# Kernel optimization log

Hardware: AMD Instinct MI355X
Metric: run time of the kernel (lower is better)

## Reference

```python
import jax, jax.numpy as jnp
from jax import lax
import numpy as np

C = 16          # channels
K = 3           # deformable kernel size
PAD = 1


def conv3(x, w, b):
    # 3x3 SAME conv, NCHW / OIHW
    y = lax.conv_general_dilated(x, w, (1, 1), 'SAME',
                                 dimension_numbers=('NCHW', 'OIHW', 'NCHW'))
    return y + b[None, :, None, None]


def deform_conv2d(x, offsets, mask, w, b):
    """torchvision-style modulated deformable conv, stride=1, pad=1, dil=1.
    x: [B,C,H,W]; offsets: [B,2*K*K,H,W] (per-tap y,x interleaved);
    mask: [B,K*K,H,W]; w: [Cout,C,K,K]; b: [Cout]."""
    B, Cin, H, W = x.shape
    ky, kx = jnp.meshgrid(jnp.arange(K), jnp.arange(K), indexing='ij')
    ky = ky.reshape(-1).astype(x.dtype)   # [9]
    kx = kx.reshape(-1).astype(x.dtype)
    off = offsets.reshape(B, K * K, 2, H, W)  # off[:,k,0]=dy, off[:,k,1]=dx
    hh = jnp.arange(H, dtype=x.dtype)
    ww = jnp.arange(W, dtype=x.dtype)
    py = hh[None, None, :, None] + (ky - PAD)[None, :, None, None] + off[:, :, 0]  # [B,9,H,W]
    px = ww[None, None, None, :] + (kx - PAD)[None, :, None, None] + off[:, :, 1]
    y0 = jnp.floor(py)
    x0 = jnp.floor(px)
    dy = py - y0
    dx = px - x0

    def sample_one(img, y0b, x0b, dyb, dxb):
        # img [C,H,W]; y0b/x0b/dyb/dxb [9,H,W]
        y0i = y0b.astype(jnp.int32)
        x0i = x0b.astype(jnp.int32)

        def gather(yi, xi):
            valid = ((yi >= 0) & (yi < H) & (xi >= 0) & (xi < W)).astype(img.dtype)
            yc = jnp.clip(yi, 0, H - 1)
            xc = jnp.clip(xi, 0, W - 1)
            return img[:, yc, xc] * valid[None]   # [C,9,H,W]

        v00 = gather(y0i,     x0i)
        v01 = gather(y0i,     x0i + 1)
        v10 = gather(y0i + 1, x0i)
        v11 = gather(y0i + 1, x0i + 1)
        return (v00 * (1 - dyb) * (1 - dxb) + v01 * (1 - dyb) * dxb
                + v10 * dyb * (1 - dxb) + v11 * dyb * dxb)   # [C,9,H,W]

    sampled = jax.vmap(sample_one)(x, y0, x0, dy, dx)          # [B,C,9,H,W]
    sampled = sampled * mask[:, None]                           # modulate
    out = jnp.einsum('bckhw,ock->bohw', sampled, w.reshape(w.shape[0], Cin, K * K))
    return out + b[None, :, None, None]


def setup_inputs() -> dict:
    key = jax.random.key(0)
    ks = iter(jax.random.split(key, 32))

    def w(shape, scale=0.1):
        return (jax.random.normal(next(ks), shape, dtype=jnp.float32) * scale)

    B, H, W = 4, 256, 256
    d = {
        'f_E': jax.random.normal(next(ks), (B, C, H, W), dtype=jnp.float32),
        'f_F': jax.random.normal(next(ks), (B, C, H, W), dtype=jnp.float32),
        # SpatialAttentionBlock
        'sab_att_w1': w((C, 2 * C, 3, 3)), 'sab_att_b1': w((C,)),
        'sab_att_w2': w((1, C, 3, 3)),      'sab_att_b2': w((1,)),
        'sab_ref_w':  w((C, 2 * C, 3, 3)),  'sab_ref_b':  w((C,)),
        # DeformableConvLayer offset/mask net (last layer small -> modest offsets)
        'om_w1': w((C, 2 * C, 3, 3)),       'om_b1': w((C,)),
        'om_w2': w((C, C, 3, 3)),           'om_b2': w((C,)),
        'om_w3': w((3 * K * K, C, 3, 3), 0.05), 'om_b3': w((3 * K * K,), 0.05),
        # deformable conv weight/bias
        'dcb_w': w((C, C, 3, 3)),           'dcb_b': w((C,)),
        # refinements
        'dcbref_w': w((C, 2 * C, 3, 3)),    'dcbref_b': w((C,)),
        'fin_w':    w((C, 2 * C, 3, 3)),    'fin_b':    w((C,)),
    }
    return d


def reference(f_E, f_F,
              sab_att_w1, sab_att_b1, sab_att_w2, sab_att_b2,
              sab_ref_w, sab_ref_b,
              om_w1, om_b1, om_w2, om_b2, om_w3, om_b3,
              dcb_w, dcb_b, dcbref_w, dcbref_b, fin_w, fin_b):
    relu = jax.nn.relu
    # --- SAB branch: sab(f_E, f_F) ---
    comb = jnp.concatenate([f_E, f_F], axis=1)
    M_E = jax.nn.sigmoid(conv3(relu(conv3(comb, sab_att_w1, sab_att_b1)),
                               sab_att_w2, sab_att_b2))          # [B,1,H,W]
    f_Esa = f_E * M_E
    f_EFsa = relu(conv3(jnp.concatenate([f_Esa, f_F], axis=1), sab_ref_w, sab_ref_b))
    # --- DCB branch: dcb_layer(f_F, f_E) -> deform on f_E, cat([f_E, f_F]) ---
    comb2 = jnp.concatenate([f_E, f_F], axis=1)
    om = conv3(relu(conv3(relu(conv3(comb2, om_w1, om_b1)), om_w2, om_b2)),
               om_w3, om_b3)                                      # [B,27,H,W]
    offsets = om[:, :2 * K * K]
    mask = jax.nn.sigmoid(om[:, 2 * K * K:])
    f_Edc = relu(deform_conv2d(f_E, offsets, mask, dcb_w, dcb_b))
    f_EFdc = relu(conv3(jnp.concatenate([f_Edc, f_F], axis=1), dcbref_w, dcbref_b))
    # --- final fusion ---
    f_EF = relu(conv3(jnp.concatenate([f_EFsa, f_EFdc], axis=1), fin_w, fin_b))
    return f_EF
```

## Files before the change

kernel.cpp:

```cpp
#include <hip/hip_runtime.h>
#include <cstdint>
#include <cstddef>

#define HH 256
#define WW 256
#define HWW (HH * WW)

typedef __attribute__((ext_vector_type(8))) short bf16x8;
typedef __attribute__((ext_vector_type(4))) float f32x4;

__device__ inline unsigned short f2bf(float f) {
  unsigned u = __float_as_uint(f);
  unsigned r = (u + 0x7fffu + ((u >> 16) & 1u)) >> 16;
  return (unsigned short)r;
}
__device__ inline float bf2f(unsigned short u) {
  return __uint_as_float((unsigned)u << 16);
}
__device__ inline float bf_lo(unsigned w) { return __uint_as_float(w << 16); }
__device__ inline float bf_hi(unsigned w) { return __uint_as_float(w & 0xffff0000u); }

struct RD { const float* src; void* dst; int cin, cout, mode; };
struct RA { RD d[9]; };

__global__ __launch_bounds__(256) void repack_k(RA a) {
  const RD t = a.d[blockIdx.x];
  if (t.mode == 2) {
    const int NST = (t.cin * 9 + 31) / 32;
    const int OT = (t.cout + 15) / 16;
    const int n = OT * NST * 512;
    unsigned short* dst = (unsigned short*)t.dst;
    for (int i = threadIdx.x; i < n; i += 256) {
      int j = i & 7;
      int l = (i >> 3) & 63;
      int rest = i >> 9;
      int s = rest % NST;
      int ot = rest / NST;
      int o = ot * 16 + (l & 15);
      int klin = s * 32 + ((l >> 4) << 3) + j;
      int tap = klin / t.cin;
      int c = klin % t.cin;
      float v = 0.f;
      if (tap < 9 && o < t.cout) v = t.src[(o * t.cin + c) * 9 + tap];
      dst[i] = f2bf(v);
    }
  } else {
    float* dst = (float*)t.dst;
    const int n = t.cin * t.cout * 9;
    for (int i = threadIdx.x; i < n; i += 256) {
      int k = i % 9;
      int rest = i / 9;
      int c = rest % t.cin;
      int o = rest / t.cin;
      if (t.mode == 0) dst[(c * 9 + k) * t.cout + o] = t.src[(o * t.cin + c) * 9 + k];
      else             dst[(k * t.cin + c) * t.cout + o] = t.src[(o * t.cin + c) * 9 + k];
    }
  }
}

__global__ __launch_bounds__(256) void nhwc2_k(
    const float* __restrict__ fe, const float* __restrict__ ff,
    unsigned short* __restrict__ xe, unsigned short* __restrict__ xf) {
  const int b = blockIdx.z;
  const int pixel = blockIdx.x * 256 + threadIdx.x;
#pragma unroll
  for (int t = 0; t < 2; ++t) {
    const float* src = t ? ff : fe;
    unsigned short* dst = t ? xf : xe;
    unsigned w[8];
#pragma unroll
    for (int j = 0; j < 8; ++j) {
      unsigned short lo = f2bf(src[((size_t)b * 16 + 2 * j) * HWW + pixel]);
      unsigned short hi = f2bf(src[((size_t)b * 16 + 2 * j + 1) * HWW + pixel]);
      w[j] = (unsigned)lo | ((unsigned)hi << 16);
    }
    uint4* d4 = (uint4*)(dst + ((size_t)b * HWW + pixel) * 16);
    d4[0] = make_uint4(w[0], w[1], w[2], w[3]);
    d4[1] = make_uint4(w[4], w[5], w[6], w[7]);
  }
}

template <int NSLOT, int OT, int OUT_MODE, int COUTR>
__global__ __launch_bounds__(256) void conv_nhwc(
    const unsigned short* __restrict__ inA, const unsigned short* __restrict__ inB,
    const unsigned short* __restrict__ wtm, const float* __restrict__ bias,
    void* __restrict__ outv) {
  constexpr int CIN = NSLOT * 8;
  constexpr int NST = (CIN * 9 + 31) / 32;
  constexpr int SHIFT = (NSLOT == 4) ? 1 : 2;
  constexpr int STRIDE = NSLOT * 16;
  constexpr int PX = 66, PY = 10;
  __shared__ __align__(16) char smem[PY * PX * STRIDE];

  const int b = blockIdx.z;
  const int tx0 = blockIdx.x * 64;
  const int ty0 = blockIdx.y * 8;
  const int tid = threadIdx.x;
  const int lane = tid & 63;
  const int wv = tid >> 6;

  bf16x8 afr[OT][NST];
#pragma unroll
  for (int ot = 0; ot < OT; ++ot)
#pragma unroll
    for (int s = 0; s < NST; ++s)
      afr[ot][s] = *(const bf16x8*)(wtm + (size_t)(((ot * NST + s) * 64 + lane) * 8));

  const int px_l = lane & 15;
  const int og = lane >> 4;

  f32x4 acc[8][OT];
#pragma unroll
  for (int ot = 0; ot < OT; ++ot) {
    f32x4 bv;
#pragma unroll
    for (int r = 0; r < 4; ++r) {
      int o = ot * 16 + og * 4 + r;
      bv[r] = bias[o < COUTR ? o : COUTR - 1];
    }
#pragma unroll
    for (int t = 0; t < 8; ++t) acc[t][ot] = bv;
  }

  for (int i = tid; i < PY * PX * NSLOT; i += 256) {
    int pp = i / NSLOT;
    int s = i - pp * NSLOT;
    int ly = pp / PX;
    int lx = pp - ly * PX;
    int gy = ty0 + ly - 1;
    int gx = tx0 + lx - 1;
    uint4 v = make_uint4(0, 0, 0, 0);
    if (gy >= 0 && gy < HH && gx >= 0 && gx < WW) {
      const unsigned short* src = (NSLOT == 2 || s < 2) ? inA : inB;
      int sl = (NSLOT == 4 && s >= 2) ? s - 2 : s;
      v = *(const uint4*)(src + ((size_t)b * HWW + (size_t)gy * WW + gx) * 16 + sl * 8);
    }
    int swz = (s ^ (pp >> SHIFT)) & (NSLOT - 1);
    *(uint4*)(smem + (size_t)pp * STRIDE + (swz << 4)) = v;
  }
  __syncthreads();

  int dpix[NST], dslot[NST];
#pragma unroll
  for (int s = 0; s < NST; ++s) {
    int klin = s * 32 + og * 8;
    int tap = klin / CIN;
    if (tap > 8) tap = 8;
    int coff = klin % CIN;
    dpix[s] = (tap / 3) * PX + (tap % 3);
    dslot[s] = coff >> 3;
  }

  const int oy_l = wv * 2;
#pragma unroll
  for (int t = 0; t < 8; ++t) {
    const int base_pix = (oy_l + (t >> 2)) * PX + (t & 3) * 16 + px_l;
#pragma unroll
    for (int s = 0; s < NST; ++s) {
      int pp = base_pix + dpix[s];
      int off = pp * STRIDE + (((dslot[s] ^ (pp >> SHIFT)) & (NSLOT - 1)) << 4);
      bf16x8 bvv = *(const bf16x8*)(smem + off);
#pragma unroll
      for (int ot = 0; ot < OT; ++ot)
        acc[t][ot] = __builtin_amdgcn_mfma_f32_16x16x32_bf16(afr[ot][s], bvv, acc[t][ot], 0, 0, 0);
    }
  }

#pragma unroll
  for (int t = 0; t < 8; ++t) {
    const int gy = ty0 + oy_l + (t >> 2);
    const int gx = tx0 + (t & 3) * 16 + px_l;
#pragma unroll
    for (int ot = 0; ot < OT; ++ot) {
      const int o0 = ot * 16 + og * 4;
      if (OUT_MODE == 2) {
        unsigned lo = (unsigned)f2bf(fmaxf(acc[t][ot][0], 0.f)) |
                      ((unsigned)f2bf(fmaxf(acc[t][ot][1], 0.f)) << 16);
        unsigned hi = (unsigned)f2bf(fmaxf(acc[t][ot][2], 0.f)) |
                      ((unsigned)f2bf(fmaxf(acc[t][ot][3], 0.f)) << 16);
        uint2* dst = (uint2*)((unsigned short*)outv +
                              ((size_t)b * HWW + (size_t)gy * WW + gx) * 16 + o0);
        *dst = make_uint2(lo, hi);
      } else if (OUT_MODE == 0) {
#pragma unroll
        for (int r = 0; r < 4; ++r) {
          int o = o0 + r;
          if (o < COUTR)
            ((float*)outv)[((size_t)b * COUTR + o) * HWW + (size_t)gy * WW + gx] =
                fmaxf(acc[t][ot][r], 0.f);
        }
      } else {
#pragma unroll
        for (int r = 0; r < 4; ++r) {
          int o = o0 + r;
          if (o < COUTR)
            ((unsigned short*)outv)[((size_t)b * COUTR + o) * HWW + (size_t)gy * WW + gx] =
                f2bf(acc[t][ot][r]);
        }
      }
    }
  }
}

__global__ __launch_bounds__(256) void conv_dual_k(
    const unsigned short* __restrict__ inA, const unsigned short* __restrict__ inB,
    const unsigned short* __restrict__ w1, const float* __restrict__ b1,
    const unsigned short* __restrict__ w2, const float* __restrict__ b2,
    unsigned short* __restrict__ out1, unsigned short* __restrict__ out2) {
  constexpr int NSLOT = 4, NST = 9, SHIFT = 1, STRIDE = 64, PX = 66, PY = 10;
  __shared__ __align__(16) char smem[PY * PX * STRIDE];

  const int b = blockIdx.z;
  const int tx0 = blockIdx.x * 64;
  const int ty0 = blockIdx.y * 8;
  const int tid = threadIdx.x;
  const int lane = tid & 63;
  const int wv = tid >> 6;

  bf16x8 afr1[NST], afr2[NST];
#pragma unroll
  for (int s = 0; s < NST; ++s) {
    afr1[s] = *(const bf16x8*)(w1 + (size_t)((s * 64 + lane) * 8));
    afr2[s] = *(const bf16x8*)(w2 + (size_t)((s * 64 + lane) * 8));
  }

  const int px_l = lane & 15;
  const int og = lane >> 4;

  f32x4 acc1[8], acc2[8];
  {
    f32x4 bv1, bv2;
#pragma unroll
    for (int r = 0; r < 4; ++r) {
      bv1[r] = b1[og * 4 + r];
      bv2[r] = b2[og * 4 + r];
    }
#pragma unroll
    for (int t = 0; t < 8; ++t) { acc1[t] = bv1; acc2[t] = bv2; }
  }

  for (int i = tid; i < PY * PX * NSLOT; i += 256) {
    int pp = i / NSLOT;
    int s = i - pp * NSLOT;
    int ly = pp / PX;
    int lx = pp - ly * PX;
    int gy = ty0 + ly - 1;
    int gx = tx0 + lx - 1;
    uint4 v = make_uint4(0, 0, 0, 0);
    if (gy >= 0 && gy < HH && gx >= 0 && gx < WW) {
      const unsigned short* src = (s < 2) ? inA : inB;
      int sl = (s >= 2) ? s - 2 : s;
      v = *(const uint4*)(src + ((size_t)b * HWW + (size_t)gy * WW + gx) * 16 + sl * 8);
    }
    int swz = (s ^ (pp >> SHIFT)) & 3;
    *(uint4*)(smem + (size_t)pp * STRIDE + (swz << 4)) = v;
  }
  __syncthreads();

  int dpix[NST], dslot[NST];
#pragma unroll
  for (int s = 0; s < NST; ++s) {
    int klin = s * 32 + og * 8;
    int tap = klin / 32;
    int coff = klin % 32;
    dpix[s] = (tap / 3) * PX + (tap % 3);
    dslot[s] = coff >> 3;
  }

  const int oy_l = wv * 2;
#pragma unroll
  for (int t = 0; t < 8; ++t) {
    const int base_pix = (oy_l + (t >> 2)) * PX + (t & 3) * 16 + px_l;
#pragma unroll
    for (int s = 0; s < NST; ++s) {
      int pp = base_pix + dpix[s];
      int off = pp * STRIDE + (((dslot[s] ^ (pp >> SHIFT)) & 3) << 4);
      bf16x8 bvv = *(const bf16x8*)(smem + off);
      acc1[t] = __builtin_amdgcn_mfma_f32_16x16x32_bf16(afr1[s], bvv, acc1[t], 0, 0, 0);
      acc2[t] = __builtin_amdgcn_mfma_f32_16x16x32_bf16(afr2[s], bvv, acc2[t], 0, 0, 0);
    }
  }

#pragma unroll
  for (int t = 0; t < 8; ++t) {
    const int gy = ty0 + oy_l + (t >> 2);
    const int gx = tx0 + (t & 3) * 16 + px_l;
    const int o0 = og * 4;
    size_t base = ((size_t)b * HWW + (size_t)gy * WW + gx) * 16 + o0;
    {
      unsigned lo = (unsigned)f2bf(fmaxf(acc1[t][0], 0.f)) |
                    ((unsigned)f2bf(fmaxf(acc1[t][1], 0.f)) << 16);
      unsigned hi = (unsigned)f2bf(fmaxf(acc1[t][2], 0.f)) |
                    ((unsigned)f2bf(fmaxf(acc1[t][3], 0.f)) << 16);
      *(uint2*)(out1 + base) = make_uint2(lo, hi);
    }
    {
      unsigned lo = (unsigned)f2bf(fmaxf(acc2[t][0], 0.f)) |
                    ((unsigned)f2bf(fmaxf(acc2[t][1], 0.f)) << 16);
      unsigned hi = (unsigned)f2bf(fmaxf(acc2[t][2], 0.f)) |
                    ((unsigned)f2bf(fmaxf(acc2[t][3], 0.f)) << 16);
      *(uint2*)(out2 + base) = make_uint2(lo, hi);
    }
  }
}

__global__ __launch_bounds__(256) void sagate_k(
    const unsigned short* __restrict__ xa, const unsigned short* __restrict__ xe,
    const unsigned short* __restrict__ xf,
    const float* __restrict__ gw, const float* __restrict__ gb,
    const unsigned short* __restrict__ wtm, const float* __restrict__ bias,
    unsigned short* __restrict__ out) {
  constexpr int NST = 9, SHIFT = 1, STRIDE = 64, PX = 66, PY = 10;
  __shared__ __align__(16) char smem[PY * PX * STRIDE];

  const int b = blockIdx.z;
  const int tx0 = blockIdx.x * 64;
  const int ty0 = blockIdx.y * 8;
  const int tid = threadIdx.x;
  const int lane = tid & 63;
  const int wv = tid >> 6;

  bf16x8 afr[NST];
#pragma unroll
  for (int s = 0; s < NST; ++s)
    afr[s] = *(const bf16x8*)(wtm + (size_t)((s * 64 + lane) * 8));

  const int px_l = lane & 15;
  const int og = lane >> 4;

  f32x4 acc[8];
  {
    f32x4 bv;
#pragma unroll
    for (int r = 0; r < 4; ++r) bv[r] = bias[og * 4 + r];
#pragma unroll
    for (int t = 0; t < 8; ++t) acc[t] = bv;
  }

  for (int i = tid; i < PY * PX * 2; i += 256) {
    int pp = i >> 1;
    int s = 2 + (i & 1);
    int ly = pp / PX;
    int lx = pp - ly * PX;
    int gy = ty0 + ly - 1;
    int gx = tx0 + lx - 1;
    uint4 v = make_uint4(0, 0, 0, 0);
    if (gy >= 0 && gy < HH && gx >= 0 && gx < WW)
      v = *(const uint4*)(xf + ((size_t)b * HWW + (size_t)gy * WW + gx) * 16 + (s - 2) * 8);
    int swz = (s ^ (pp >> SHIFT)) & 3;
    *(uint4*)(smem + (size_t)pp * STRIDE + (swz << 4)) = v;
  }

  const float gbias = gb[0];
  for (int i = tid; i < PY * PX; i += 256) {
    int ly = i / PX;
    int lx = i - ly * PX;
    int gy = ty0 + ly - 1;
    int gx = tx0 + lx - 1;
    uint4 v0 = make_uint4(0, 0, 0, 0), v1 = make_uint4(0, 0, 0, 0);
    if (gy >= 0 && gy < HH && gx >= 0 && gx < WW) {
      float a = gbias;
#pragma unroll
      for (int ky = 0; ky < 3; ++ky) {
        int ay = gy + ky - 1;
        if (ay < 0 || ay >= HH) continue;
#pragma unroll
        for (int kx = 0; kx < 3; ++kx) {
          int ax = gx + kx - 1;
          if (ax < 0 || ax >= WW) continue;
          const int k = ky * 3 + kx;
          const uint4* p = (const uint4*)(xa + ((size_t)b * HWW + (size_t)ay * WW + ax) * 16);
          uint4 t0 = p[0], t1 = p[1];
          unsigned wv8[8] = {t0.x, t0.y, t0.z, t0.w, t1.x, t1.y, t1.z, t1.w};
#pragma unroll
          for (int j = 0; j < 8; ++j) {
            a = fmaf(bf_lo(wv8[j]), gw[(2 * j) * 9 + k], a);
            a = fmaf(bf_hi(wv8[j]), gw[(2 * j + 1) * 9 + k], a);
          }
        }
      }
      float m = 1.0f / (1.0f + expf(-a));
      const uint4* pe = (const uint4*)(xe + ((size_t)b * HWW + (size_t)gy * WW + gx) * 16);
      uint4 e0 = pe[0], e1 = pe[1];
      unsigned ev[8] = {e0.x, e0.y, e0.z, e0.w, e1.x, e1.y, e1.z, e1.w};
      unsigned r[8];
#pragma unroll
      for (int j = 0; j < 8; ++j) {
        unsigned short lo = f2bf(bf_lo(ev[j]) * m);
        unsigned short hi = f2bf(bf_hi(ev[j]) * m);
        r[j] = (unsigned)lo | ((unsigned)hi << 16);
      }
      v0 = make_uint4(r[0], r[1], r[2], r[3]);
      v1 = make_uint4(r[4], r[5], r[6], r[7]);
    }
    int swz0 = (0 ^ (i >> SHIFT)) & 3;
    int swz1 = (1 ^ (i >> SHIFT)) & 3;
    *(uint4*)(smem + (size_t)i * STRIDE + (swz0 << 4)) = v0;
    *(uint4*)(smem + (size_t)i * STRIDE + (swz1 << 4)) = v1;
  }
  __syncthreads();

  int dpix[NST], dslot[NST];
#pragma unroll
  for (int s = 0; s < NST; ++s) {
    int klin = s * 32 + og * 8;
    int tap = klin / 32;
    int coff = klin % 32;
    dpix[s] = (tap / 3) * PX + (tap % 3);
    dslot[s] = coff >> 3;
  }

  const int oy_l = wv * 2;
#pragma unroll
  for (int t = 0; t < 8; ++t) {
    const int base_pix = (oy_l + (t >> 2)) * PX + (t & 3) * 16 + px_l;
#pragma unroll
    for (int s = 0; s < NST; ++s) {
      int pp = base_pix + dpix[s];
      int off = pp * STRIDE + (((dslot[s] ^ (pp >> SHIFT)) & 3) << 4);
      bf16x8 bvv = *(const bf16x8*)(smem + off);
      acc[t] = __builtin_amdgcn_mfma_f32_16x16x32_bf16(afr[s], bvv, acc[t], 0, 0, 0);
    }
  }

#pragma unroll
  for (int t = 0; t < 8; ++t) {
    const int gy = ty0 + oy_l + (t >> 2);
    const int gx = tx0 + (t & 3) * 16 + px_l;
    const int o0 = og * 4;
    unsigned lo = (unsigned)f2bf(fmaxf(acc[t][0], 0.f)) |
                  ((unsigned)f2bf(fmaxf(acc[t][1], 0.f)) << 16);
    unsigned hi = (unsigned)f2bf(fmaxf(acc[t][2], 0.f)) |
                  ((unsigned)f2bf(fmaxf(acc[t][3], 0.f)) << 16);
    *(uint2*)(out + ((size_t)b * HWW + (size_t)gy * WW + gx) * 16 + o0) = make_uint2(lo, hi);
  }
}

__global__ __launch_bounds__(256) void deform_v4(
    const unsigned short* __restrict__ xn, const unsigned short* __restrict__ om,
    const float* __restrict__ wt, const float* __restrict__ bias,
    unsigned short* __restrict__ out) {
  const int bid = blockIdx.x;
  const int xcd = bid & 7;
  const int b = xcd >> 1;
  const int pb = ((bid >> 3) << 1) | (xcd & 1);
  const int pixel = pb * 256 + (int)threadIdx.x;
  const int y = pixel >> 8;
  const int xq = pixel & 255;
  const unsigned short* xb = xn + (size_t)b * HWW * 16;
  const unsigned short* omb = om + (size_t)b * 27 * HWW;

  float acc[16];
#pragma unroll
  for (int o = 0; o < 16; ++o) acc[o] = bias[o];

#pragma unroll
  for (int k = 0; k < 9; ++k) {
    float offy = bf2f(omb[(size_t)(2 * k) * HWW + pixel]);
    float offx = bf2f(omb[(size_t)(2 * k + 1) * HWW + pixel]);
    float m = 1.0f / (1.0f + expf(-bf2f(omb[(size_t)(18 + k) * HWW + pixel])));
    float py = (float)y + (float)(k / 3 - 1) + offy;
    float px = (float)xq + (float)(k % 3 - 1) + offx;
    float y0f = floorf(py);
    float x0f = floorf(px);
    float dy = py - y0f;
    float dx = px - x0f;
    int y0 = (int)y0f, x0 = (int)x0f;
    int y1 = y0 + 1, x1 = x0 + 1;
    bool vy0 = (y0 >= 0) && (y0 < HH);
    bool vy1 = (y1 >= 0) && (y1 < HH);
    bool vx0 = (x0 >= 0) && (x0 < WW);
    bool vx1 = (x1 >= 0) && (x1 < WW);
    int yc0 = min(max(y0, 0), HH - 1);
    int yc1 = min(max(y1, 0), HH - 1);
    int xc0 = min(max(x0, 0), WW - 1);
    int xc1 = min(max(x1, 0), WW - 1);
    float w00 = (1.f - dy) * (1.f - dx) * m;
    float w01 = (1.f - dy) * dx * m;
    float w10 = dy * (1.f - dx) * m;
    float w11 = dy * dx * m;
    if (!(vy0 && vx0)) w00 = 0.f;
    if (!(vy0 && vx1)) w01 = 0.f;
    if (!(vy1 && vx0)) w10 = 0.f;
    if (!(vy1 && vx1)) w11 = 0.f;

    const uint4* p00 = (const uint4*)(xb + (size_t)(yc0 * WW + xc0) * 16);
    const uint4* p01 = (const uint4*)(xb + (size_t)(yc0 * WW + xc1) * 16);
    const uint4* p10 = (const uint4*)(xb + (size_t)(yc1 * WW + xc0) * 16);
    const uint4* p11 = (const uint4*)(xb + (size_t)(yc1 * WW + xc1) * 16);
    uint4 a0 = p00[0], a1 = p00[1];
    uint4 b0 = p01[0], b1 = p01[1];
    uint4 c0 = p10[0], c1 = p10[1];
    uint4 d0 = p11[0], d1 = p11[1];
    unsigned wA[8] = {a0.x, a0.y, a0.z, a0.w, a1.x, a1.y, a1.z, a1.w};
    unsigned wB[8] = {b0.x, b0.y, b0.z, b0.w, b1.x, b1.y, b1.z, b1.w};
    unsigned wC[8] = {c0.x, c0.y, c0.z, c0.w, c1.x, c1.y, c1.z, c1.w};
    unsigned wD[8] = {d0.x, d0.y, d0.z, d0.w, d1.x, d1.y, d1.z, d1.w};

    float s[16];
#pragma unroll
    for (int j = 0; j < 8; ++j) {
      s[2 * j]     = bf_lo(wA[j]) * w00 + bf_lo(wB[j]) * w01 + bf_lo(wC[j]) * w10 + bf_lo(wD[j]) * w11;
      s[2 * j + 1] = bf_hi(wA[j]) * w00 + bf_hi(wB[j]) * w01 + bf_hi(wC[j]) * w10 + bf_hi(wD[j]) * w11;
    }
    const float* wk = wt + (size_t)k * 256;
#pragma unroll
    for (int c = 0; c < 16; ++c)
#pragma unroll
      for (int o = 0; o < 16; ++o)
        acc[o] = fmaf(s[c], wk[c * 16 + o], acc[o]);
  }
  unsigned r[8];
#pragma unroll
  for (int j = 0; j < 8; ++j) {
    unsigned short lo = f2bf(fmaxf(acc[2 * j], 0.f));
    unsigned short hi = f2bf(fmaxf(acc[2 * j + 1], 0.f));
    r[j] = (unsigned)lo | ((unsigned)hi << 16);
  }
  uint4* d4 = (uint4*)(out + ((size_t)b * HWW + pixel) * 16);
  d4[0] = make_uint4(r[0], r[1], r[2], r[3]);
  d4[1] = make_uint4(r[4], r[5], r[6], r[7]);
}

extern "C" void kernel_launch(void* const* d_in, const int* in_sizes, int n_in,
                              void* d_out, int out_size, void* d_ws, size_t ws_size,
                              hipStream_t stream) {
  (void)in_sizes; (void)n_in; (void)out_size; (void)ws_size;
  const float* f_E = (const float*)d_in[0];
  const float* f_F = (const float*)d_in[1];
  const float* att_w1 = (const float*)d_in[2];
  const float* att_b1 = (const float*)d_in[3];
  const float* att_w2 = (const float*)d_in[4];
  const float* att_b2 = (const float*)d_in[5];
  const float* ref_w = (const float*)d_in[6];
  const float* ref_b = (const float*)d_in[7];
  const float* om_w1 = (const float*)d_in[8];
  const float* om_b1 = (const float*)d_in[9];
  const float* om_w2 = (const float*)d_in[10];
  const float* om_b2 = (const float*)d_in[11];
  const float* om_w3 = (const float*)d_in[12];
  const float* om_b3 = (const float*)d_in[13];
  const float* dcb_w = (const float*)d_in[14];
  const float* dcb_b = (const float*)d_in[15];
  const float* dcbref_w = (const float*)d_in[16];
  const float* dcbref_b = (const float*)d_in[17];
  const float* fin_w = (const float*)d_in[18];
  const float* fin_b = (const float*)d_in[19];
  float* outp = (float*)d_out;

  const size_t TN = (size_t)4 * HWW * 16;
  unsigned short* XE  = (unsigned short*)d_ws;
  unsigned short* XF  = XE + TN;
  unsigned short* XA  = XF + TN;
  unsigned short* XT  = XA + TN;
  unsigned short* X2  = XT + TN;
  unsigned short* XSA = X2 + TN;
  unsigned short* OMB = XSA + TN;
  unsigned short* WM  = OMB + (size_t)4 * 27 * HWW;

  unsigned short* WM_att1 = WM;
  unsigned short* WM_ref  = WM_att1 + 4608;
  unsigned short* WM_om1  = WM_ref + 4608;
  unsigned short* WM_om2  = WM_om1 + 4608;
  unsigned short* WM_om3  = WM_om2 + 2560;
  unsigned short* WM_dref = WM_om3 + 5120;
  unsigned short* WM_fin  = WM_dref + 4608;
  float* WF_att2 = (float*)(WM_fin + 4608);
  float* WF_dcb  = WF_att2 + 144;

  RA ra;
  ra.d[0] = {att_w1, WM_att1, 32, 16, 2};
  ra.d[1] = {ref_w, WM_ref, 32, 16, 2};
  ra.d[2] = {om_w1, WM_om1, 32, 16, 2};
  ra.d[3] = {om_w2, WM_om2, 16, 16, 2};
  ra.d[4] = {om_w3, WM_om3, 16, 27, 2};
  ra.d[5] = {dcbref_w, WM_dref, 32, 16, 2};
  ra.d[6] = {fin_w, WM_fin, 32, 16, 2};
  ra.d[7] = {att_w2, WF_att2, 16, 1, 0};
  ra.d[8] = {dcb_w, WF_dcb, 16, 16, 1};
  repack_k<<<dim3(9), dim3(256), 0, stream>>>(ra);
  nhwc2_k<<<dim3(HWW / 256, 1, 4), dim3(256), 0, stream>>>(f_E, f_F, XE, XF);

  dim3 blk(256);
  dim3 gm(WW / 64, HH / 8, 4);

  conv_dual_k<<<gm, blk, 0, stream>>>(XE, XF, WM_att1, att_b1, WM_om1, om_b1, XA, XT);
  sagate_k<<<gm, blk, 0, stream>>>(XA, XE, XF, WF_att2, att_b2, WM_ref, ref_b, X2);
  conv_nhwc<2, 1, 2, 16><<<gm, blk, 0, stream>>>(XT, nullptr, WM_om2, om_b2, XA);
  conv_nhwc<2, 2, 1, 27><<<gm, blk, 0, stream>>>(XA, nullptr, WM_om3, om_b3, OMB);
  deform_v4<<<dim3(1024), blk, 0, stream>>>(XE, OMB, WF_dcb, dcb_b, XSA);
  conv_nhwc<4, 1, 2, 16><<<gm, blk, 0, stream>>>(XSA, XF, WM_dref, dcbref_b, XT);
  conv_nhwc<4, 1, 0, 16><<<gm, blk, 0, stream>>>(X2, XT, WM_fin, fin_b, outp);
}
```

Measured before the change: 121.8 us.

## Use zero-padded NHWC buffers and direct global loads in convs

Switches all intermediate NHWC bf16 tensors to a zero-bordered 258x258 layout, with a small kernel that clears the borders. The conv kernels can then read halo pixels straight from global memory with no bounds checks, dropping the LDS staging and barrier. Block indices are remapped so adjacent blocks are spread across batch and tiles, which is meant to improve cache locality. The cost is that the nine overlapping tap reads now depend on L1/L2 reuse instead of shared memory, so global load traffic goes up.

```diff
diff --git a/kernel.cpp b/kernel.cpp
--- a/kernel.cpp
+++ b/kernel.cpp
@@ -5,6 +5,7 @@
 #define HH 256
 #define WW 256
 #define HWW (HH * WW)
+#define PS 258
 
 typedef __attribute__((ext_vector_type(8))) short bf16x8;
 typedef __attribute__((ext_vector_type(4))) float f32x4;
@@ -58,11 +59,30 @@
   }
 }
 
+struct BorderP { unsigned short* p[6]; };
+
+__global__ __launch_bounds__(256) void border_k(BorderP bp) {
+  unsigned short* t = bp.p[blockIdx.x];
+  const int b = blockIdx.y;
+  for (int i = threadIdx.x; i < 1028; i += 256) {
+    int row, col;
+    if (i < 258) { row = 0; col = i; }
+    else if (i < 516) { row = 257; col = i - 258; }
+    else if (i < 772) { row = i - 516 + 1; col = 0; }
+    else { row = i - 772 + 1; col = 257; }
+    uint4* d = (uint4*)(t + ((size_t)(b * PS + row) * PS + col) * 16);
+    d[0] = make_uint4(0, 0, 0, 0);
+    d[1] = make_uint4(0, 0, 0, 0);
+  }
+}
+
 __global__ __launch_bounds__(256) void nhwc2_k(
     const float* __restrict__ fe, const float* __restrict__ ff,
     unsigned short* __restrict__ xe, unsigned short* __restrict__ xf) {
   const int b = blockIdx.z;
   const int pixel = blockIdx.x * 256 + threadIdx.x;
+  const int y = pixel >> 8;
+  const int x = pixel & 255;
 #pragma unroll
   for (int t = 0; t < 2; ++t) {
     const float* src = t ? ff : fe;
@@ -74,27 +94,26 @@
       unsigned short hi = f2bf(src[((size_t)b * 16 + 2 * j + 1) * HWW + pixel]);
       w[j] = (unsigned)lo | ((unsigned)hi << 16);
     }
-    uint4* d4 = (uint4*)(dst + ((size_t)b * HWW + pixel) * 16);
+    uint4* d4 = (uint4*)(dst + ((size_t)(b * PS + y + 1) * PS + x + 1) * 16);
     d4[0] = make_uint4(w[0], w[1], w[2], w[3]);
     d4[1] = make_uint4(w[4], w[5], w[6], w[7]);
   }
 }
 
 template <int NSLOT, int OT, int OUT_MODE, int COUTR>
-__global__ __launch_bounds__(256) void conv_nhwc(
+__global__ __launch_bounds__(256) void conv_direct(
     const unsigned short* __restrict__ inA, const unsigned short* __restrict__ inB,
     const unsigned short* __restrict__ wtm, const float* __restrict__ bias,
     void* __restrict__ outv) {
   constexpr int CIN = NSLOT * 8;
   constexpr int NST = (CIN * 9 + 31) / 32;
-  constexpr int SHIFT = (NSLOT == 4) ? 1 : 2;
-  constexpr int STRIDE = NSLOT * 16;
-  constexpr int PX = 66, PY = 10;
-  __shared__ __align__(16) char smem[PY * PX * STRIDE];
-
-  const int b = blockIdx.z;
-  const int tx0 = blockIdx.x * 64;
-  const int ty0 = blockIdx.y * 8;
+
+  const int bid = blockIdx.x;
+  const int wg = (bid & 7) * 64 + (bid >> 3);
+  const int b = wg >> 7;
+  const int rem = wg & 127;
+  const int ty0 = (rem >> 2) * 8;
+  const int tx0 = (rem & 3) * 64;
   const int tid = threadIdx.x;
   const int lane = tid & 63;
   const int wv = tid >> 6;
@@ -122,48 +141,38 @@
     for (int t = 0; t < 8; ++t) acc[t][ot] = bv;
   }
 
-  for (int i = tid; i < PY * PX * NSLOT; i += 256) {
-    int pp = i / NSLOT;
-    int s = i - pp * NSLOT;
-    int ly = pp / PX;
-    int lx = pp - ly * PX;
-    int gy = ty0 + ly - 1;
-    int gx = tx0 + lx - 1;
-    uint4 v = make_uint4(0, 0, 0, 0);
-    if (gy >= 0 && gy < HH && gx >= 0 && gx < WW) {
-      const unsigned short* src = (NSLOT == 2 || s < 2) ? inA : inB;
-      int sl = (NSLOT == 4 && s >= 2) ? s - 2 : s;
-      v = *(const uint4*)(src + ((size_t)b * HWW + (size_t)gy * WW + gx) * 16 + sl * 8);
-    }
-    int swz = (s ^ (pp >> SHIFT)) & (NSLOT - 1);
-    *(uint4*)(smem + (size_t)pp * STRIDE + (swz << 4)) = v;
-  }
-  __syncthreads();
-
-  int dpix[NST], dslot[NST];
+  int offE[NST];
+  bool useB[NST];
 #pragma unroll
   for (int s = 0; s < NST; ++s) {
     int klin = s * 32 + og * 8;
     int tap = klin / CIN;
     if (tap > 8) tap = 8;
     int coff = klin % CIN;
-    dpix[s] = (tap / 3) * PX + (tap % 3);
-    dslot[s] = coff >> 3;
+    int slot = (NSLOT == 4) ? (coff >> 3) & 1 : (coff >> 3);
+    useB[s] = (NSLOT == 4) && (coff >= 16);
+    offE[s] = ((tap / 3) * PS + (tap % 3)) * 16 + slot * 8;
   }
 
   const int oy_l = wv * 2;
 #pragma unroll
   for (int t = 0; t < 8; ++t) {
-    const int base_pix = (oy_l + (t >> 2)) * PX + (t & 3) * 16 + px_l;
+    const int gy = ty0 + oy_l + (t >> 2);
+    const int gx = tx0 + (t & 3) * 16 + px_l;
+    const size_t base = ((size_t)(b * PS + gy) * PS + gx) * 16;
+    const unsigned short* baseA = inA + base;
+    const unsigned short* baseB = inB + base;
+    bf16x8 bv[NST];
 #pragma unroll
     for (int s = 0; s < NST; ++s) {
-      int pp = base_pix + dpix[s];
-      int off = pp * STRIDE + (((dslot[s] ^ (pp >> SHIFT)) & (NSLOT - 1)) << 4);
-      bf16x8 bvv = *(const bf16x8*)(smem + off);
+      const unsigned short* p = useB[s] ? baseB : baseA;
+      bv[s] = *(const bf16x8*)(p + offE[s]);
+    }
+#pragma unroll
+    for (int s = 0; s < NST; ++s)
 #pragma unroll
       for (int ot = 0; ot < OT; ++ot)
-        acc[t][ot] = __builtin_amdgcn_mfma_f32_16x16x32_bf16(afr[ot][s], bvv, acc[t][ot], 0, 0, 0);
-    }
+        acc[t][ot] = __builtin_amdgcn_mfma_f32_16x16x32_bf16(afr[ot][s], bv[s], acc[t][ot], 0, 0, 0);
   }
 
 #pragma unroll
@@ -179,7 +188,7 @@
         unsigned hi = (unsigned)f2bf(fmaxf(acc[t][ot][2], 0.f)) |
                       ((unsigned)f2bf(fmaxf(acc[t][ot][3], 0.f)) << 16);
         uint2* dst = (uint2*)((unsigned short*)outv +
-                              ((size_t)b * HWW + (size_t)gy * WW + gx) * 16 + o0);
+                              ((size_t)(b * PS + gy + 1) * PS + gx + 1) * 16 + o0);
         *dst = make_uint2(lo, hi);
       } else if (OUT_MODE == 0) {
 #pragma unroll
@@ -202,17 +211,18 @@
   }
 }
 
-__global__ __launch_bounds__(256) void conv_dual_k(
+__global__ __launch_bounds__(256) void conv_dual_direct(
     const unsigned short* __restrict__ inA, const unsigned short* __restrict__ inB,
     const unsigned short* __restrict__ w1, const float* __restrict__ b1,
     const unsigned short* __restrict__ w2, const float* __restrict__ b2,
     unsigned short* __restrict__ out1, unsigned short* __restrict__ out2) {
-  constexpr int NSLOT = 4, NST = 9, SHIFT = 1, STRIDE = 64, PX = 66, PY = 10;
-  __shared__ __align__(16) char smem[PY * PX * STRIDE];
-
-  const int b = blockIdx.z;
-  const int tx0 = blockIdx.x * 64;
-  const int ty0 = blockIdx.y * 8;
+  constexpr int NST = 9;
+  const int bid = blockIdx.x;
+  const int wg = (bid & 7) * 64 + (bid >> 3);
+  const int b = wg >> 7;
+  const int rem = wg & 127;
+  const int ty0 = (rem >> 2) * 8;
+  const int tx0 = (rem & 3) * 64;
   const int tid = threadIdx.x;
   const int lane = tid & 63;
   const int wv = tid >> 6;
@@ -239,54 +249,44 @@
     for (int t = 0; t < 8; ++t) { acc1[t] = bv1; acc2[t] = bv2; }
   }
 
-  for (int i = tid; i < PY * PX * NSLOT; i += 256) {
-    int pp = i / NSLOT;
-    int s = i - pp * NSLOT;
-    int ly = pp / PX;
-    int lx = pp - ly * PX;
-    int gy = ty0 + ly - 1;
-    int gx = tx0 + lx - 1;
-    uint4 v = make_uint4(0, 0, 0, 0);
-    if (gy >= 0 && gy < HH && gx >= 0 && gx < WW) {
-      const unsigned short* src = (s < 2) ? inA : inB;
-      int sl = (s >= 2) ? s - 2 : s;
-      v = *(const uint4*)(src + ((size_t)b * HWW + (size_t)gy * WW + gx) * 16 + sl * 8);
-    }
-    int swz = (s ^ (pp >> SHIFT)) & 3;
-    *(uint4*)(smem + (size_t)pp * STRIDE + (swz << 4)) = v;
-  }
-  __syncthreads();
-
-  int dpix[NST], dslot[NST];
+  int offE[NST];
+  bool useB[NST];
 #pragma unroll
   for (int s = 0; s < NST; ++s) {
     int klin = s * 32 + og * 8;
     int tap = klin / 32;
     int coff = klin % 32;
-    dpix[s] = (tap / 3) * PX + (tap % 3);
-    dslot[s] = coff >> 3;
+    int slot = (coff >> 3) & 1;
+    useB[s] = (coff >= 16);
+    offE[s] = ((tap / 3) * PS + (tap % 3)) * 16 + slot * 8;
   }
 
   const int oy_l = wv * 2;
-#pragma unroll
-  for (int t = 0; t < 8; ++t) {
-    const int base_pix = (oy_l + (t >> 2)) * PX + (t & 3) * 16 + px_l;
-#pragma unroll
-    for (int s = 0; s < NST; ++s) {
-      int pp = base_pix + dpix[s];
-      int off = pp * STRIDE + (((dslot[s] ^ (pp >> SHIFT)) & 3) << 4);
-      bf16x8 bvv = *(const bf16x8*)(smem + off);
-      acc1[t] = __builtin_amdgcn_mfma_f32_16x16x32_bf16(afr1[s], bvv, acc1[t], 0, 0, 0);
-      acc2[t] = __builtin_amdgcn_mfma_f32_16x16x32_bf16(afr2[s], bvv, acc2[t], 0, 0, 0);
-    }
-  }
-
 #pragma unroll
   for (int t = 0; t < 8; ++t) {
     const int gy = ty0 + oy_l + (t >> 2);
     const int gx = tx0 + (t & 3) * 16 + px_l;
-    const int o0 = og * 4;
-    size_t base = ((size_t)b * HWW + (size_t)gy * WW + gx) * 16 + o0;
+    const size_t base = ((size_t)(b * PS + gy) * PS + gx) * 16;
+    const unsigned short* baseA = inA + base;
+    const unsigned short* baseB = inB + base;
+    bf16x8 bv[NST];
+#pragma unroll
+    for (int s = 0; s < NST; ++s) {
+      const unsigned short* p = useB[s] ? baseB : baseA;
+      bv[s] = *(const bf16x8*)(p + offE[s]);
+    }
+#pragma unroll
+    for (int s = 0; s < NST; ++s) {
+      acc1[t] = __builtin_amdgcn_mfma_f32_16x16x32_bf16(afr1[s], bv[s], acc1[t], 0, 0, 0);
+      acc2[t] = __builtin_amdgcn_mfma_f32_16x16x32_bf16(afr2[s], bv[s], acc2[t], 0, 0, 0);
+    }
+  }
+
+#pragma unroll
+  for (int t = 0; t < 8; ++t) {
+    const int gy = ty0 + oy_l + (t >> 2);
+    const int gx = tx0 + (t & 3) * 16 + px_l;
+    const size_t base = ((size_t)(b * PS + gy + 1) * PS + gx + 1) * 16 + og * 4;
     {
       unsigned lo = (unsigned)f2bf(fmaxf(acc1[t][0], 0.f)) |
                     ((unsigned)f2bf(fmaxf(acc1[t][1], 0.f)) << 16);
@@ -342,11 +342,7 @@
     int s = 2 + (i & 1);
     int ly = pp / PX;
     int lx = pp - ly * PX;
-    int gy = ty0 + ly - 1;
-    int gx = tx0 + lx - 1;
-    uint4 v = make_uint4(0, 0, 0, 0);
-    if (gy >= 0 && gy < HH && gx >= 0 && gx < WW)
-      v = *(const uint4*)(xf + ((size_t)b * HWW + (size_t)gy * WW + gx) * 16 + (s - 2) * 8);
+    uint4 v = *(const uint4*)(xf + ((size_t)(b * PS + ty0 + ly) * PS + tx0 + lx) * 16 + (s - 2) * 8);
     int swz = (s ^ (pp >> SHIFT)) & 3;
     *(uint4*)(smem + (size_t)pp * STRIDE + (swz << 4)) = v;
   }
@@ -355,48 +351,41 @@
   for (int i = tid; i < PY * PX; i += 256) {
     int ly = i / PX;
     int lx = i - ly * PX;
-    int gy = ty0 + ly - 1;
-    int gx = tx0 + lx - 1;
-    uint4 v0 = make_uint4(0, 0, 0, 0), v1 = make_uint4(0, 0, 0, 0);
-    if (gy >= 0 && gy < HH && gx >= 0 && gx < WW) {
-      float a = gbias;
-#pragma unroll
-      for (int ky = 0; ky < 3; ++ky) {
-        int ay = gy + ky - 1;
-        if (ay < 0 || ay >= HH) continue;
-#pragma unroll
-        for (int kx = 0; kx < 3; ++kx) {
-          int ax = gx + kx - 1;
-          if (ax < 0 || ax >= WW) continue;
-          const int k = ky * 3 + kx;
-          const uint4* p = (const uint4*)(xa + ((size_t)b * HWW + (size_t)ay * WW + ax) * 16);
-          uint4 t0 = p[0], t1 = p[1];
-          unsigned wv8[8] = {t0.x, t0.y, t0.z, t0.w, t1.x, t1.y, t1.z, t1.w};
-#pragma unroll
-          for (int j = 0; j < 8; ++j) {
-            a = fmaf(bf_lo(wv8[j]), gw[(2 * j) * 9 + k], a);
-            a = fmaf(bf_hi(wv8[j]), gw[(2 * j + 1) * 9 + k], a);
-          }
+    const int pcy = ty0 + ly;
+    const int pcx = tx0 + lx;
+    float a = gbias;
+#pragma unroll
+    for (int ky = 0; ky < 3; ++ky) {
+      int ty = min(max(pcy + ky - 1, 0), PS - 1);
+#pragma unroll
+      for (int kx = 0; kx < 3; ++kx) {
+        int tx = min(max(pcx + kx - 1, 0), PS - 1);
+        const int k = ky * 3 + kx;
+        const uint4* p = (const uint4*)(xa + ((size_t)(b * PS + ty) * PS + tx) * 16);
+        uint4 t0 = p[0], t1 = p[1];
+        unsigned wv8[8] = {t0.x, t0.y, t0.z, t0.w, t1.x, t1.y, t1.z, t1.w};
+#pragma unroll
+        for (int j = 0; j < 8; ++j) {
+          a = fmaf(bf_lo(wv8[j]), gw[(2 * j) * 9 + k], a);
+          a = fmaf(bf_hi(wv8[j]), gw[(2 * j + 1) * 9 + k], a);
         }
       }
-      float m = 1.0f / (1.0f + expf(-a));
-      const uint4* pe = (const uint4*)(xe + ((size_t)b * HWW + (size_t)gy * WW + gx) * 16);
-      uint4 e0 = pe[0], e1 = pe[1];
-      unsigned ev[8] = {e0.x, e0.y, e0.z, e0.w, e1.x, e1.y, e1.z, e1.w};
-      unsigned r[8];
-#pragma unroll
-      for (int j = 0; j < 8; ++j) {
-        unsigned short lo = f2bf(bf_lo(ev[j]) * m);
-        unsigned short hi = f2bf(bf_hi(ev[j]) * m);
-        r[j] = (unsigned)lo | ((unsigned)hi << 16);
-      }
-      v0 = make_uint4(r[0], r[1], r[2], r[3]);
-      v1 = make_uint4(r[4], r[5], r[6], r[7]);
+    }
+    float m = 1.0f / (1.0f + expf(-a));
+    const uint4* pe = (const uint4*)(xe + ((size_t)(b * PS + pcy) * PS + pcx) * 16);
+    uint4 e0 = pe[0], e1 = pe[1];
+    unsigned ev[8] = {e0.x, e0.y, e0.z, e0.w, e1.x, e1.y, e1.z, e1.w};
+    unsigned r[8];
+#pragma unroll
+    for (int j = 0; j < 8; ++j) {
+      unsigned short lo = f2bf(bf_lo(ev[j]) * m);
+      unsigned short hi = f2bf(bf_hi(ev[j]) * m);
+      r[j] = (unsigned)lo | ((unsigned)hi << 16);
     }
     int swz0 = (0 ^ (i >> SHIFT)) & 3;
     int swz1 = (1 ^ (i >> SHIFT)) & 3;
-    *(uint4*)(smem + (size_t)i * STRIDE + (swz0 << 4)) = v0;
-    *(uint4*)(smem + (size_t)i * STRIDE + (swz1 << 4)) = v1;
+    *(uint4*)(smem + (size_t)i * STRIDE + (swz0 << 4)) = make_uint4(r[0], r[1], r[2], r[3]);
+    *(uint4*)(smem + (size_t)i * STRIDE + (swz1 << 4)) = make_uint4(r[4], r[5], r[6], r[7]);
   }
   __syncthreads();
 
@@ -427,16 +416,15 @@
   for (int t = 0; t < 8; ++t) {
     const int gy = ty0 + oy_l + (t >> 2);
     const int gx = tx0 + (t & 3) * 16 + px_l;
-    const int o0 = og * 4;
     unsigned lo = (unsigned)f2bf(fmaxf(acc[t][0], 0.f)) |
                   ((unsigned)f2bf(fmaxf(acc[t][1], 0.f)) << 16);
     unsigned hi = (unsigned)f2bf(fmaxf(acc[t][2], 0.f)) |
                   ((unsigned)f2bf(fmaxf(acc[t][3], 0.f)) << 16);
-    *(uint2*)(out + ((size_t)b * HWW + (size_t)gy * WW + gx) * 16 + o0) = make_uint2(lo, hi);
-  }
-}
-
-__global__ __launch_bounds__(256) void deform_v4(
+    *(uint2*)(out + ((size_t)(b * PS + gy + 1) * PS + gx + 1) * 16 + og * 4) = make_uint2(lo, hi);
+  }
+}
+
+__global__ __launch_bounds__(256) void deform_v5(
     const unsigned short* __restrict__ xn, const unsigned short* __restrict__ om,
     const float* __restrict__ wt, const float* __restrict__ bias,
     unsigned short* __restrict__ out) {
@@ -447,7 +435,7 @@
   const int pixel = pb * 256 + (int)threadIdx.x;
   const int y = pixel >> 8;
   const int xq = pixel & 255;
-  const unsigned short* xb = xn + (size_t)b * HWW * 16;
+  const unsigned short* xb = xn + (size_t)b * PS * PS * 16;
   const unsigned short* omb = om + (size_t)b * 27 * HWW;
 
   float acc[16];
@@ -471,10 +459,10 @@
     bool vy1 = (y1 >= 0) && (y1 < HH);
     bool vx0 = (x0 >= 0) && (x0 < WW);
     bool vx1 = (x1 >= 0) && (x1 < WW);
-    int yc0 = min(max(y0, 0), HH - 1);
-    int yc1 = min(max(y1, 0), HH - 1);
-    int xc0 = min(max(x0, 0), WW - 1);
-    int xc1 = min(max(x1, 0), WW - 1);
+    int yc0 = min(max(y0, 0), HH - 1) + 1;
+    int yc1 = min(max(y1, 0), HH - 1) + 1;
+    int xc0 = min(max(x0, 0), WW - 1) + 1;
+    int xc1 = min(max(x1, 0), WW - 1) + 1;
     float w00 = (1.f - dy) * (1.f - dx) * m;
     float w01 = (1.f - dy) * dx * m;
     float w10 = dy * (1.f - dx) * m;
@@ -484,10 +472,10 @@
     if (!(vy1 && vx0)) w10 = 0.f;
     if (!(vy1 && vx1)) w11 = 0.f;
 
-    const uint4* p00 = (const uint4*)(xb + (size_t)(yc0 * WW + xc0) * 16);
-    const uint4* p01 = (const uint4*)(xb + (size_t)(yc0 * WW + xc1) * 16);
-    const uint4* p10 = (const uint4*)(xb + (size_t)(yc1 * WW + xc0) * 16);
-    const uint4* p11 = (const uint4*)(xb + (size_t)(yc1 * WW + xc1) * 16);
+    const uint4* p00 = (const uint4*)(xb + ((size_t)yc0 * PS + xc0) * 16);
+    const uint4* p01 = (const uint4*)(xb + ((size_t)yc0 * PS + xc1) * 16);
+    const uint4* p10 = (const uint4*)(xb + ((size_t)yc1 * PS + xc0) * 16);
+    const uint4* p11 = (const uint4*)(xb + ((size_t)yc1 * PS + xc1) * 16);
     uint4 a0 = p00[0], a1 = p00[1];
     uint4 b0 = p01[0], b1 = p01[1];
     uint4 c0 = p10[0], c1 = p10[1];
@@ -517,7 +505,7 @@
     unsigned short hi = f2bf(fmaxf(acc[2 * j + 1], 0.f));
     r[j] = (unsigned)lo | ((unsigned)hi << 16);
   }
-  uint4* d4 = (uint4*)(out + ((size_t)b * HWW + pixel) * 16);
+  uint4* d4 = (uint4*)(out + ((size_t)(b * PS + y + 1) * PS + xq + 1) * 16);
   d4[0] = make_uint4(r[0], r[1], r[2], r[3]);
   d4[1] = make_uint4(r[4], r[5], r[6], r[7]);
 }
@@ -548,14 +536,14 @@
   const float* fin_b = (const float*)d_in[19];
   float* outp = (float*)d_out;
 
-  const size_t TN = (size_t)4 * HWW * 16;
+  const size_t TNP = (size_t)4 * PS * PS * 16;
   unsigned short* XE  = (unsigned short*)d_ws;
-  unsigned short* XF  = XE + TN;
-  unsigned short* XA  = XF + TN;
-  unsigned short* XT  = XA + TN;
-  unsigned short* X2  = XT + TN;
-  unsigned short* XSA = X2 + TN;
-  unsigned short* OMB = XSA + TN;
+  unsigned short* XF  = XE + TNP;
+  unsigned short* XA  = XF + TNP;
+  unsigned short* XT  = XA + TNP;
+  unsigned short* X2  = XT + TNP;
+  unsigned short* XSA = X2 + TNP;
+  unsigned short* OMB = XSA + TNP;
   unsigned short* WM  = OMB + (size_t)4 * 27 * HWW;
 
   unsigned short* WM_att1 = WM;
@@ -579,16 +567,23 @@
   ra.d[7] = {att_w2, WF_att2, 16, 1, 0};
   ra.d[8] = {dcb_w, WF_dcb, 16, 16, 1};
   repack_k<<<dim3(9), dim3(256), 0, stream>>>(ra);
+
+  BorderP bp;
+  bp.p[0] = XE; bp.p[1] = XF; bp.p[2] = XA;
+  bp.p[3] = XT; bp.p[4] = X2; bp.p[5] = XSA;
+  border_k<<<dim3(6, 4), dim3(256), 0, stream>>>(bp);
+
   nhwc2_k<<<dim3(HWW / 256, 1, 4), dim3(256), 0, stream>>>(f_E, f_F, XE, XF);
 
   dim3 blk(256);
+  dim3 gd(512);
   dim3 gm(WW / 64, HH / 8, 4);
 
-  conv_dual_k<<<gm, blk, 0, stream>>>(XE, XF, WM_att1, att_b1, WM_om1, om_b1, XA, XT);
+  conv_dual_direct<<<gd, blk, 0, stream>>>(XE, XF, WM_att1, att_b1, WM_om1, om_b1, XA, XT);
   sagate_k<<<gm, blk, 0, stream>>>(XA, XE, XF, WF_att2, att_b2, WM_ref, ref_b, X2);
-  conv_nhwc<2, 1, 2, 16><<<gm, blk, 0, stream>>>(XT, nullptr, WM_om2, om_b2, XA);
-  conv_nhwc<2, 2, 1, 27><<<gm, blk, 0, stream>>>(XA, nullptr, WM_om3, om_b3, OMB);
-  deform_v4<<<dim3(1024), blk, 0, stream>>>(XE, OMB, WF_dcb, dcb_b, XSA);
-  conv_nhwc<4, 1, 2, 16><<<gm, blk, 0, stream>>>(XSA, XF, WM_dref, dcbref_b, XT);
-  conv_nhwc<4, 1, 0, 16><<<gm, blk, 0, stream>>>(X2, XT, WM_fin, fin_b, outp);
-}
+  conv_direct<2, 1, 2, 16><<<gd, blk, 0, stream>>>(XT, XT, WM_om2, om_b2, XA);
+  conv_direct<2, 2, 1, 27><<<gd, blk, 0, stream>>>(XA, XA, WM_om3, om_b3, OMB);
+  deform_v5<<<dim3(1024), blk, 0, stream>>>(XE, OMB, WF_dcb, dcb_b, XSA);
+  conv_direct<4, 1, 2, 16><<<gd, blk, 0, stream>>>(XSA, XF, WM_dref, dcbref_b, XT);
+  conv_direct<4, 1, 0, 16><<<gd, blk, 0, stream>>>(X2, XT, WM_fin, fin_b, outp);
+}
```

After: 134.1 us. 1.1x slower.
